# Kernel optimization log

Hardware: AMD Instinct MI355X
Metric: run time of the kernel (lower is better)

Reference implementation:

```python
import jax, jax.numpy as jnp
import numpy as np

B, NC, D, H, W = 2, 5, 96, 160, 160


def setup_inputs() -> dict:
    key = jax.random.key(0)
    k1, k2, k3 = jax.random.split(key, 3)
    source_logits = jax.random.normal(k1, (B, NC, D, H, W), dtype=jnp.float32)
    target_logits = jax.random.normal(k2, (B, NC, D, H, W), dtype=jnp.float32)
    gt = jax.random.randint(k3, (B, 1, D, H, W), 0, NC, dtype=jnp.int64)
    return {"source_logits": source_logits, "target_logits": target_logits, "gt": gt}


def reference(source_logits, target_logits, gt):
    temperature = 2.0
    eps = 1e-6
    n_class = source_logits.shape[1]
    batch = source_logits.shape[0]

    g = gt[:, 0]  # [B, D, H, W]
    # one-hot over classes: [K, B, D, H, W] (K = n_class segment ids)
    onehot = (g[None] == jnp.arange(n_class)[:, None, None, None, None]).astype(source_logits.dtype)
    # total voxel count per class over the whole batch (matches torch.sum(gt == i))
    nvox = jnp.sum(onehot, axis=(1, 2, 3, 4))  # [K]

    # per-class, per-batch, per-channel masked sums: single pass instead of n_class passes
    s_sum = jnp.einsum('kbdhw,bcdhw->kbc', onehot, source_logits)  # [K, B, C]
    t_sum = jnp.einsum('kbdhw,bcdhw->kbc', onehot, target_logits)

    denom = (nvox + eps)[:, None, None]
    s_avg = s_sum[:, :, 1:] / denom  # [K, B, C-1] (channel 0 dropped as in original)
    t_avg = t_sum[:, :, 1:] / denom

    s_lp = jax.nn.log_softmax(s_avg / temperature, axis=-1)
    t_lp = jax.nn.log_softmax(t_avg / temperature, axis=-1)

    # KLDivLoss(reduction='batchmean', log_target=True): sum(exp(t)*(t-s)) / batch
    kl_st = jnp.sum(jnp.exp(t_lp) * (t_lp - s_lp), axis=(1, 2)) / batch  # per class
    kl_ts = jnp.sum(jnp.exp(s_lp) * (s_lp - t_lp), axis=(1, 2)) / batch

    return jnp.mean((kl_st + kl_ts) / 2.0)
```

## Files before the change

### kernel.cpp

```cpp
#include <hip/hip_runtime.h>

#define NCLASS 5
#define NB 2
#define VOX (96*160*160)
#define V4  (VOX/4)

#define WS_FLOATS 110

__global__ __launch_bounds__(256)
void kd_partial(const float* __restrict__ src, const float* __restrict__ tgt,
                const int* __restrict__ gt, float* __restrict__ ws)
{
    const int nbPerB = gridDim.x >> 1;
    const int b      = blockIdx.x / nbPerB;
    const int blk    = blockIdx.x - b * nbPerB;

    const float* sb = src + (size_t)b * NCLASS * VOX;
    const float* tb = tgt + (size_t)b * NCLASS * VOX;
    const int*   gb = gt  + (size_t)b * VOX;

    float accS[NCLASS][NCLASS];
    float accT[NCLASS][NCLASS];
    float cnt[NCLASS];
    #pragma unroll
    for (int k = 0; k < NCLASS; ++k) {
        cnt[k] = 0.f;
        #pragma unroll
        for (int c = 0; c < NCLASS; ++c) { accS[k][c] = 0.f; accT[k][c] = 0.f; }
    }

    const int tid    = blk * 256 + threadIdx.x;
    const int stride = nbPerB * 256;

    for (int i = tid; i < V4; i += stride) {
        const int4 g4 = ((const int4*)gb)[i];
        float4 s4[NCLASS], t4[NCLASS];
        #pragma unroll
        for (int c = 0; c < NCLASS; ++c) {
            s4[c] = ((const float4*)(sb + (size_t)c * VOX))[i];
            t4[c] = ((const float4*)(tb + (size_t)c * VOX))[i];
        }
        #define DO_VOX(GK, COMP) {                                           \
            const int kv = (GK);                                             \
            _Pragma("unroll")                                                \
            for (int kk = 0; kk < NCLASS; ++kk) {                            \
                const float m = (kv == kk) ? 1.0f : 0.0f;                    \
                cnt[kk] += m;                                                \
                _Pragma("unroll")                                            \
                for (int c = 0; c < NCLASS; ++c) {                           \
                    accS[kk][c] = fmaf(m, s4[c].COMP, accS[kk][c]);          \
                    accT[kk][c] = fmaf(m, t4[c].COMP, accT[kk][c]);          \
                }                                                            \
            }                                                                \
        }
        DO_VOX(g4.x, x)
        DO_VOX(g4.y, y)
        DO_VOX(g4.z, z)
        DO_VOX(g4.w, w)
        #undef DO_VOX
    }

    __shared__ float lacc[55];
    const int lane = threadIdx.x & 63;
    if (threadIdx.x < 55) lacc[threadIdx.x] = 0.f;
    __syncthreads();

    #define WAVE_RED(VAL, IDX) {                                             \
        float v_ = (VAL);                                                    \
        _Pragma("unroll")                                                    \
        for (int off_ = 32; off_; off_ >>= 1) v_ += __shfl_xor(v_, off_);    \
        if (lane == 0) atomicAdd(&lacc[(IDX)], v_);                          \
    }
    #pragma unroll
    for (int k = 0; k < NCLASS; ++k) {
        #pragma unroll
        for (int c = 0; c < NCLASS; ++c) {
            WAVE_RED(accS[k][c], k * 5 + c);
            WAVE_RED(accT[k][c], 25 + k * 5 + c);
        }
        WAVE_RED(cnt[k], 50 + k);
    }
    #undef WAVE_RED
    __syncthreads();

    if (threadIdx.x < 55) {
        const int i = threadIdx.x;
        int gidx;
        if (i < 25)       gidx = b * 25 + i;
        else if (i < 50)  gidx = 50 + b * 25 + (i - 25);
        else              gidx = 100 + b * 5 + (i - 50);
        atomicAdd(&ws[gidx], lacc[i]);
    }
}

__global__ void kd_final(const float* __restrict__ ws, float* __restrict__ out)
{
    if (threadIdx.x == 0 && blockIdx.x == 0) {
        double total = 0.0;
        for (int k = 0; k < NCLASS; ++k) {
            const double denom = (double)ws[100 + 0 * 5 + k]
                               + (double)ws[100 + 1 * 5 + k] + 1e-6;
            for (int b = 0; b < NB; ++b) {
                double sa[4], ta[4];
                for (int c = 0; c < 4; ++c) {
                    sa[c] = ((double)ws[(b * 5 + k) * 5 + (c + 1)] / denom) * 0.5;
                    ta[c] = ((double)ws[50 + (b * 5 + k) * 5 + (c + 1)] / denom) * 0.5;
                }
                double ms = sa[0], mt = ta[0];
                for (int c = 1; c < 4; ++c) {
                    if (sa[c] > ms) ms = sa[c];
                    if (ta[c] > mt) mt = ta[c];
                }
                double es = 0.0, et = 0.0;
                for (int c = 0; c < 4; ++c) { es += exp(sa[c] - ms); et += exp(ta[c] - mt); }
                const double lses = ms + log(es);
                const double lset = mt + log(et);
                for (int c = 0; c < 4; ++c) {
                    const double slp = sa[c] - lses;
                    const double tlp = ta[c] - lset;
                    total += exp(tlp) * (tlp - slp) + exp(slp) * (slp - tlp);
                }
            }
        }
        out[0] = (float)(total / 20.0);
    }
}

extern "C" void kernel_launch(void* const* d_in, const int* in_sizes, int n_in,
                              void* d_out, int out_size, void* d_ws, size_t ws_size,
                              hipStream_t stream)
{
    const float* src = (const float*)d_in[0];
    const float* tgt = (const float*)d_in[1];
    const int*   gt  = (const int*)d_in[2];
    float* out = (float*)d_out;
    float* ws  = (float*)d_ws;

    hipMemsetAsync(ws, 0, WS_FLOATS * sizeof(float), stream);
    kd_partial<<<dim3(1024), dim3(256), 0, stream>>>(src, tgt, gt, ws);
    kd_final<<<dim3(1), dim3(64), 0, stream>>>(ws, out);
}
```

Baseline: 260.0 us.

## Stagger channel plane reads, spread atomics over slots, parallelize final reduction

The main loop now handles one channel at a time and offsets each channel's index by a prime stagger. Different channel planes are read at different addresses at the same moment, which is meant to avoid memory channel or bank camping from the large power-of-two-like plane strides. The gt value is reloaded for each channel, which adds redundant int4 loads. Global atomics are spread over 64 workspace slots to cut contention. The grid is doubled to 2048 blocks, and the final kernel is parallelized with wave shuffles instead of a single serial thread.

```diff
diff --git a/kernel.cpp b/kernel.cpp
--- a/kernel.cpp
+++ b/kernel.cpp
@@ -4,8 +4,10 @@
 #define NB 2
 #define VOX (96*160*160)
 #define V4  (VOX/4)
+#define SLOTS 64
+#define VALS  110
+#define STAGP 1271
 
-#define WS_FLOATS 110
 
 __global__ __launch_bounds__(256)
 void kd_partial(const float* __restrict__ src, const float* __restrict__ tgt,
@@ -33,31 +35,35 @@
     const int stride = nbPerB * 256;
 
     for (int i = tid; i < V4; i += stride) {
-        const int4 g4 = ((const int4*)gb)[i];
-        float4 s4[NCLASS], t4[NCLASS];
         #pragma unroll
         for (int c = 0; c < NCLASS; ++c) {
-            s4[c] = ((const float4*)(sb + (size_t)c * VOX))[i];
-            t4[c] = ((const float4*)(tb + (size_t)c * VOX))[i];
+            int ic = i + c * STAGP;
+            if (ic >= V4) ic -= V4;
+            const int4   g4 = ((const int4*)gb)[ic];
+            const float4 s4 = ((const float4*)(sb + (size_t)c * VOX))[ic];
+            const float4 t4 = ((const float4*)(tb + (size_t)c * VOX))[ic];
+
+            #define ACC_COMP(GX, SX, TX)                                     \
+                { _Pragma("unroll")                                          \
+                  for (int kk = 0; kk < NCLASS; ++kk) {                      \
+                      const float m = ((GX) == kk) ? 1.0f : 0.0f;            \
+                      accS[kk][c] = fmaf(m, (SX), accS[kk][c]);              \
+                      accT[kk][c] = fmaf(m, (TX), accT[kk][c]);              \
+                  } }
+            ACC_COMP(g4.x, s4.x, t4.x)
+            ACC_COMP(g4.y, s4.y, t4.y)
+            ACC_COMP(g4.z, s4.z, t4.z)
+            ACC_COMP(g4.w, s4.w, t4.w)
+            #undef ACC_COMP
+
+            if (c == 0) {
+                #pragma unroll
+                for (int kk = 0; kk < NCLASS; ++kk) {
+                    cnt[kk] += ((g4.x == kk) ? 1.f : 0.f) + ((g4.y == kk) ? 1.f : 0.f)
+                             + ((g4.z == kk) ? 1.f : 0.f) + ((g4.w == kk) ? 1.f : 0.f);
+                }
+            }
         }
-        #define DO_VOX(GK, COMP) {                                           \
-            const int kv = (GK);                                             \
-            _Pragma("unroll")                                                \
-            for (int kk = 0; kk < NCLASS; ++kk) {                            \
-                const float m = (kv == kk) ? 1.0f : 0.0f;                    \
-                cnt[kk] += m;                                                \
-                _Pragma("unroll")                                            \
-                for (int c = 0; c < NCLASS; ++c) {                           \
-                    accS[kk][c] = fmaf(m, s4[c].COMP, accS[kk][c]);          \
-                    accT[kk][c] = fmaf(m, t4[c].COMP, accT[kk][c]);          \
-                }                                                            \
-            }                                                                \
-        }
-        DO_VOX(g4.x, x)
-        DO_VOX(g4.y, y)
-        DO_VOX(g4.z, z)
-        DO_VOX(g4.w, w)
-        #undef DO_VOX
     }
 
     __shared__ float lacc[55];
@@ -89,41 +95,49 @@
         if (i < 25)       gidx = b * 25 + i;
         else if (i < 50)  gidx = 50 + b * 25 + (i - 25);
         else              gidx = 100 + b * 5 + (i - 50);
-        atomicAdd(&ws[gidx], lacc[i]);
+        atomicAdd(&ws[(blockIdx.x & (SLOTS - 1)) * VALS + gidx], lacc[i]);
     }
 }
 
 __global__ void kd_final(const float* __restrict__ ws, float* __restrict__ out)
 {
-    if (threadIdx.x == 0 && blockIdx.x == 0) {
-        double total = 0.0;
-        for (int k = 0; k < NCLASS; ++k) {
-            const double denom = (double)ws[100 + 0 * 5 + k]
-                               + (double)ws[100 + 1 * 5 + k] + 1e-6;
-            for (int b = 0; b < NB; ++b) {
-                double sa[4], ta[4];
-                for (int c = 0; c < 4; ++c) {
-                    sa[c] = ((double)ws[(b * 5 + k) * 5 + (c + 1)] / denom) * 0.5;
-                    ta[c] = ((double)ws[50 + (b * 5 + k) * 5 + (c + 1)] / denom) * 0.5;
-                }
-                double ms = sa[0], mt = ta[0];
-                for (int c = 1; c < 4; ++c) {
-                    if (sa[c] > ms) ms = sa[c];
-                    if (ta[c] > mt) mt = ta[c];
-                }
-                double es = 0.0, et = 0.0;
-                for (int c = 0; c < 4; ++c) { es += exp(sa[c] - ms); et += exp(ta[c] - mt); }
-                const double lses = ms + log(es);
-                const double lset = mt + log(et);
-                for (int c = 0; c < 4; ++c) {
-                    const double slp = sa[c] - lses;
-                    const double tlp = ta[c] - lset;
-                    total += exp(tlp) * (tlp - slp) + exp(slp) * (slp - tlp);
-                }
-            }
-        }
-        out[0] = (float)(total / 20.0);
+    const int tid = threadIdx.x;
+    __shared__ float tot[VALS];
+
+    for (int v = tid; v < VALS; v += 64) {
+        float s = 0.f;
+        #pragma unroll 8
+        for (int slot = 0; slot < SLOTS; ++slot) s += ws[slot * VALS + v];
+        tot[v] = s;
     }
+    __syncthreads();
+
+    const int l = (tid < 40) ? tid : 0;
+    const int g = l >> 2;
+    const int k = g >> 1;
+    const int b = g & 1;
+    const int c = l & 3;
+
+    const double denom = (double)tot[100 + 0 * 5 + k]
+                       + (double)tot[100 + 1 * 5 + k] + 1e-6;
+    double sa = ((double)tot[(b * 5 + k) * 5 + (c + 1)] / denom) * 0.5;
+    double ta = ((double)tot[50 + (b * 5 + k) * 5 + (c + 1)] / denom) * 0.5;
+
+    double ms = sa, mt = ta;
+    ms = fmax(ms, __shfl_xor(ms, 1)); ms = fmax(ms, __shfl_xor(ms, 2));
+    mt = fmax(mt, __shfl_xor(mt, 1)); mt = fmax(mt, __shfl_xor(mt, 2));
+    double es = exp(sa - ms), et = exp(ta - mt);
+    es += __shfl_xor(es, 1); es += __shfl_xor(es, 2);
+    et += __shfl_xor(et, 1); et += __shfl_xor(et, 2);
+    const double slp = sa - (ms + log(es));
+    const double tlp = ta - (mt + log(et));
+
+    double term = exp(tlp) * (tlp - slp) + exp(slp) * (slp - tlp);
+    if (tid >= 40) term = 0.0;
+
+    #pragma unroll
+    for (int off = 32; off; off >>= 1) term += __shfl_xor(term, off);
+    if (tid == 0) out[0] = (float)(term / 20.0);
 }
 
 extern "C" void kernel_launch(void* const* d_in, const int* in_sizes, int n_in,
@@ -136,7 +150,7 @@
     float* out = (float*)d_out;
     float* ws  = (float*)d_ws;
 
-    hipMemsetAsync(ws, 0, WS_FLOATS * sizeof(float), stream);
-    kd_partial<<<dim3(1024), dim3(256), 0, stream>>>(src, tgt, gt, ws);
+    hipMemsetAsync(ws, 0, SLOTS * VALS * sizeof(float), stream);
+    kd_partial<<<dim3(2048), dim3(256), 0, stream>>>(src, tgt, gt, ws);
     kd_final<<<dim3(1), dim3(64), 0, stream>>>(ws, out);
 }
```

Measured after the change: 280.1 us. +7.7%, slower.
